# Performance work log

Measured on AMD Instinct MI355X. Metric: run time of the kernel, lower is better.

Reference implementation:

```python
import jax, jax.numpy as jnp
import numpy as np

N, IN_F, OUT_F, H = 8192, 256, 64, 4
NEG_SLOPE = 0.2


def setup_inputs() -> dict:
    key = jax.random.key(0)
    ks = jax.random.split(key, 8)
    inputs = jax.random.normal(ks[0], (N, IN_F), dtype=jnp.float32)
    # sparse-ish binary adjacency with self loops (sparse.softmax only sees nonzeros)
    adj = (jax.random.uniform(ks[1], (N, N)) < 0.05).astype(jnp.float32)
    idx = jnp.arange(N)
    adj = adj.at[idx, idx].set(1.0)
    stdv = 1.0 / np.sqrt(H * OUT_F)
    weight = jax.random.uniform(ks[2], (IN_F, H * OUT_F), minval=-stdv, maxval=stdv, dtype=jnp.float32)
    bias = jax.random.uniform(ks[3], (1, H * OUT_F), minval=-stdv, maxval=stdv, dtype=jnp.float32)
    # weight_u/v: stdv = 1/sqrt(size(-1)=1) = 1
    weight_u = jax.random.uniform(ks[4], (H, OUT_F, 1), minval=-1.0, maxval=1.0, dtype=jnp.float32)
    weight_v = jax.random.uniform(ks[5], (H, OUT_F, 1), minval=-1.0, maxval=1.0, dtype=jnp.float32)
    stdp = 1.0 / np.sqrt(IN_F)
    proj_w = jax.random.uniform(ks[6], (H * OUT_F, IN_F), minval=-stdp, maxval=stdp, dtype=jnp.float32)
    proj_b = jax.random.uniform(ks[7], (H * OUT_F,), minval=-stdp, maxval=stdp, dtype=jnp.float32)
    return {"inputs": inputs, "adj_mat": adj, "weight": weight, "weight_u": weight_u,
            "weight_v": weight_v, "bias": bias, "proj_w": proj_w, "proj_b": proj_b}


def reference(inputs, adj_mat, weight, weight_u, weight_v, bias, proj_w, proj_b):
    n = inputs.shape[0]
    support = (inputs @ weight).reshape(n, H, OUT_F).transpose(1, 0, 2)  # [H,N,O]
    f1 = jnp.einsum('hno,ho->hn', support, weight_u[..., 0])  # [H,N]
    f2 = jnp.einsum('hno,ho->hn', support, weight_v[..., 0])  # [H,N]
    logits = f1[:, None, :] + f2[:, :, None]                  # [H,N,N]
    w = jax.nn.leaky_relu(logits, NEG_SLOPE)
    masked = w * adj_mat                                      # adj broadcast over heads
    mask = adj_mat != 0.0
    # sparse.softmax over dim 2: softmax restricted to nonzero (edge) positions
    neg = jnp.where(mask, masked, -jnp.inf)
    m = jnp.max(neg, axis=2, keepdims=True)
    m = jnp.where(jnp.isfinite(m), m, 0.0)
    e = jnp.where(mask, jnp.exp(neg - m), 0.0)
    denom = jnp.sum(e, axis=2, keepdims=True)
    attn = e / jnp.where(denom > 0, denom, 1.0)               # [H,N,N]
    out = jnp.einsum('hnm,hmo->hno', attn, support)           # [H,N,O]
    out = out.transpose(1, 0, 2).reshape(n, H * OUT_F)
    out = out + bias
    out = out + inputs @ proj_w.T + proj_b
    return out
```

## Files before the change

### kernel.cpp

```cpp
#include <hip/hip_runtime.h>
#include <hip/hip_bf16.h>

#define N_NODES 8192
#define IN_FEAT 256
#define OUT_F   64
#define NHEAD   4
#define HF      256
#define NEG     0.2f

typedef unsigned short u16;
typedef unsigned char  u8;
typedef unsigned int   u32;
typedef unsigned long long u64;
typedef _Float16 h2    __attribute__((ext_vector_type(2)));
typedef _Float16 half8 __attribute__((ext_vector_type(8)));
typedef __attribute__((ext_vector_type(4))) float f32x4;

__global__ __launch_bounds__(256) void k_x16(const float* __restrict__ inp,
                                             _Float16* __restrict__ X16,
                                             float* __restrict__ anum,
                                             float* __restrict__ aden) {
    const int i = blockIdx.x * 256 + threadIdx.x;
    const float4 v = ((const float4*)inp)[i];
    union { _Float16 hh[4]; u64 q; } cv;
    cv.hh[0] = (_Float16)v.x; cv.hh[1] = (_Float16)v.y;
    cv.hh[2] = (_Float16)v.z; cv.hh[3] = (_Float16)v.w;
    ((u64*)X16)[i] = cv.q;
    ((float4*)anum)[i] = (float4){0.f, 0.f, 0.f, 0.f};
    if (i < 8192) ((float4*)aden)[i] = (float4){0.f, 0.f, 0.f, 0.f};
}

__global__ __launch_bounds__(256) void k_wpack(const float* __restrict__ W,
                                               const float* __restrict__ PW,
                                               _Float16* __restrict__ W16B) {
    const int w = blockIdx.x * 256 + threadIdx.x;
    const int ks = w >> 11;
    const int T  = (w >> 6) & 31;
    const int lane = w & 63;
    const int q  = lane >> 4, cc = lane & 15;
    const int n  = T * 16 + cc;
    const int k0 = ks * 32 + q * 8;
    union { _Float16 hh[8]; half8 v; } o;
    #pragma unroll
    for (int e = 0; e < 8; ++e) {
        const int k = k0 + e;
        const float s = (n < 256) ? W[k * 256 + n] : PW[(size_t)(n - 256) * 256 + k];
        o.hh[e] = (_Float16)s;
    }
    *(half8*)(W16B + (size_t)w * 8) = o.v;
}

__global__ __launch_bounds__(256) void k_bits(const float* __restrict__ adj,
                                              u64* __restrict__ gb64) {
    const int row  = blockIdx.x * 4 + (threadIdx.x >> 6);
    const int lane = threadIdx.x & 63;
    const float* ar = adj + (size_t)row * N_NODES;
    u64* gr = gb64 + (size_t)row * 128;
    #pragma unroll 1
    for (int it = 0; it < 32; ++it) {
        const int jb = it * 256;
        const float a0 = ar[jb + lane];
        const float a1 = ar[jb + 64 + lane];
        const float a2 = ar[jb + 128 + lane];
        const float a3 = ar[jb + 192 + lane];
        const u64 b0 = __ballot(a0 != 0.f);
        const u64 b1 = __ballot(a1 != 0.f);
        const u64 b2 = __ballot(a2 != 0.f);
        const u64 b3 = __ballot(a3 != 0.f);
        if (lane == 0) {
            gr[it * 4 + 0] = b0; gr[it * 4 + 1] = b1;
            gr[it * 4 + 2] = b2; gr[it * 4 + 3] = b3;
        }
    }
}

#define GROWS 16
__global__ __launch_bounds__(256) void k_gemm(
    const _Float16* __restrict__ X16,
    const _Float16* __restrict__ W16B,
    const float* __restrict__ U,
    const float* __restrict__ V,
    const float* __restrict__ Bias,
    const float* __restrict__ PB,
    _Float16* __restrict__ suppB,
    float* __restrict__ f1,
    float* __restrict__ f2,
    float* __restrict__ outp)
{
    __shared__ __align__(16) _Float16 xl[GROWS][264];
    const int n0  = blockIdx.x * GROWS;
    const int tid = threadIdx.x;
    const int wv  = tid >> 6, lane = tid & 63;
    const int col = lane & 15, quad = lane >> 4;

    {
        const int r = tid >> 4, seg = tid & 15;
        const half8* src = (const half8*)(X16 + (size_t)(n0 + r) * 256 + seg * 16);
        *(half8*)&xl[r][seg * 16]     = src[0];
        *(half8*)&xl[r][seg * 16 + 8] = src[1];
    }
    __syncthreads();

    f32x4 acc[8];
    #pragma unroll
    for (int t = 0; t < 8; ++t) acc[t] = (f32x4){0.f, 0.f, 0.f, 0.f};

    const int qo = quad * 8;
    #pragma unroll
    for (int ks = 0; ks < 8; ++ks) {
        const half8 af = *(const half8*)&xl[col][ks * 32 + qo];
        const _Float16* bb = W16B + ((size_t)(ks * 32 + wv * 8) * 64 + lane) * 8;
        #pragma unroll
        for (int t = 0; t < 8; ++t) {
            const half8 bw = *(const half8*)(bb + (size_t)t * 512);
            acc[t] = __builtin_amdgcn_mfma_f32_16x16x32_f16(af, bw, acc[t], 0, 0, 0);
        }
    }

    if (wv < 2) {
        const int jbg = n0 >> 5;
        const int nlo = n0 & 31;
        #pragma unroll
        for (int t = 0; t < 8; ++t) {
            const int cg = wv * 128 + t * 16 + col;
            const int h  = cg >> 6;
            const int tp = (cg >> 4) & 3;
            #pragma unroll
            for (int reg = 0; reg < 4; ++reg) {
                const int irow = quad * 4 + reg;
                const int j31  = nlo + irow;
                const size_t word = ((size_t)(h * 256 + jbg) * 4 + tp) * 64
                                  + ((j31 >> 3) << 4) + col;
                suppB[word * 8 + (j31 & 7)] = (_Float16)acc[t][reg];
            }
        }
        float s1a[4] = {0,0,0,0}, s2a[4] = {0,0,0,0};
        float s1b[4] = {0,0,0,0}, s2b[4] = {0,0,0,0};
        #pragma unroll
        for (int t = 0; t < 8; ++t) {
            const int cg = wv * 128 + t * 16 + col;
            const float uu = U[cg], vv = V[cg];
            #pragma unroll
            for (int reg = 0; reg < 4; ++reg) {
                if (t < 4) { s1a[reg] += acc[t][reg] * uu; s2a[reg] += acc[t][reg] * vv; }
                else       { s1b[reg] += acc[t][reg] * uu; s2b[reg] += acc[t][reg] * vv; }
            }
        }
        #pragma unroll
        for (int m = 1; m < 16; m <<= 1) {
            #pragma unroll
            for (int reg = 0; reg < 4; ++reg) {
                s1a[reg] += __shfl_xor(s1a[reg], m);
                s2a[reg] += __shfl_xor(s2a[reg], m);
                s1b[reg] += __shfl_xor(s1b[reg], m);
                s2b[reg] += __shfl_xor(s2b[reg], m);
            }
        }
        if (col == 0) {
            const int hA = wv * 2, hB = wv * 2 + 1;
            #pragma unroll
            for (int reg = 0; reg < 4; ++reg) {
                const int n = n0 + quad * 4 + reg;
                f1[hA * N_NODES + n] = s1a[reg];
                f2[hA * N_NODES + n] = s2a[reg];
                f1[hB * N_NODES + n] = s1b[reg];
                f2[hB * N_NODES + n] = s2b[reg];
            }
        }
    } else {
        #pragma unroll
        for (int t = 0; t < 8; ++t) {
            const int cg = (wv - 2) * 128 + t * 16 + col;
            const float bb2 = Bias[cg] + PB[cg];
            #pragma unroll
            for (int reg = 0; reg < 4; ++reg) {
                const int irow = quad * 4 + reg;
                outp[(size_t)(n0 + irow) * HF + cg] = acc[t][reg] + bb2;
            }
        }
    }
}

__global__ __launch_bounds__(256) void k_prep(const float* __restrict__ f1,
                                              float* __restrict__ f1max,
                                              _Float16* __restrict__ EA16,
                                              _Float16* __restrict__ EB16) {
    __shared__ float red[256];
    const int h = blockIdx.x;
    float m = -1e30f;
    for (int j = threadIdx.x; j < N_NODES; j += 256)
        m = fmaxf(m, f1[h * N_NODES + j]);
    red[threadIdx.x] = m;
    __syncthreads();
    for (int s = 128; s > 0; s >>= 1) {
        if (threadIdx.x < s) red[threadIdx.x] = fmaxf(red[threadIdx.x], red[threadIdx.x + s]);
        __syncthreads();
    }
    const float fm = red[0];
    if (threadIdx.x == 0) f1max[h] = fm;
    for (int j = threadIdx.x; j < N_NODES; j += 256) {
        const float d = f1[h * N_NODES + j] - fm;
        EA16[(size_t)h * N_NODES + j] = (_Float16)__expf(d);
        EB16[(size_t)h * N_NODES + j] = (_Float16)__expf(NEG * d);
    }
}

#define TI 64
#define NSUB 4
#define JSPLIT_G 4
#define JW (N_NODES / JSPLIT_G)

__global__ __launch_bounds__(256, 3) void k_attn_mfma(
    const unsigned* __restrict__ gb32,
    const _Float16* __restrict__ suppB,
    const _Float16* __restrict__ EA16,
    const _Float16* __restrict__ EB16,
    const float* __restrict__ f2,
    const float* __restrict__ f1max,
    float* __restrict__ anum,
    float* __restrict__ aden)
{
    __shared__ __align__(16) _Float16 ea_lds[NHEAD][JW];
    __shared__ __align__(16) _Float16 eb_lds[NHEAD][JW];
    __shared__ __align__(4)  u8 abyte[TI][260];

    const int itile = blockIdx.x >> 2;
    const int jwin  = blockIdx.x & 3;
    const int i0    = itile * TI;
    const int J0    = jwin * JW;
    const int wv    = threadIdx.x >> 6;
    const int lane  = threadIdx.x & 63;
    const int col   = lane & 15;
    const int quad  = lane >> 4;

    {
        const _Float16* gea = EA16 + (size_t)wv * N_NODES + J0;
        const _Float16* geb = EB16 + (size_t)wv * N_NODES + J0;
        #pragma unroll
        for (int it = 0; it < 4; ++it) {
            const int off = it * 512 + lane * 8;
            *(float4*)&ea_lds[wv][off] = *(const float4*)(gea + off);
            *(float4*)&eb_lds[wv][off] = *(const float4*)(geb + off);
        }
    }
    #pragma unroll
    for (int rr = 0; rr < 16; ++rr) {
        const int r = (wv << 4) + rr;
        *(unsigned*)&abyte[r][lane * 4] =
            gb32[(size_t)(i0 + r) * 256 + (J0 >> 5) + lane];
    }
    __syncthreads();

    const int h = wv;
    const float fm = f1max[h];
    h2 caH[NSUB], cbH[NSUB];
    float ls[NSUB];
    #pragma unroll
    for (int s = 0; s < NSUB; ++s) {
        const float f2i = f2[(size_t)h * N_NODES + i0 + s * 16 + col];
        const float g  = fm + f2i;
        const float mi = fmaxf(g, NEG * g);
        const _Float16 ca = (_Float16)__expf(g - mi);
        const _Float16 cb = (_Float16)__expf(NEG * g - mi);
        caH[s][0] = ca; caH[s][1] = ca;
        cbH[s][0] = cb; cbH[s][1] = cb;
        ls[s] = 0.f;
    }
    const h2 ones = {(_Float16)1.0f, (_Float16)1.0f};

    const _Float16* sb = suppB + (size_t)h * 524288
                       + (size_t)(J0 >> 5) * 2048 + lane * 8;

    f32x4 acc[NSUB][4];
    #pragma unroll
    for (int s = 0; s < NSUB; ++s)
        #pragma unroll
        for (int t = 0; t < 4; ++t)
            acc[s][t] = (f32x4){0.f, 0.f, 0.f, 0.f};

    const int qo = quad << 3;

    #pragma unroll 2
    for (int jb = 0; jb < JW; jb += 32) {
        const int jl = jb + qo;
        const _Float16* fp = sb + (size_t)(jb >> 5) * 2048;
        const half8 bv0 = *(const half8*)(fp);
        const half8 bv1 = *(const half8*)(fp + 512);
        const half8 bv2 = *(const half8*)(fp + 1024);
        const half8 bv3 = *(const half8*)(fp + 1536);

        union { half8 v; h2 pr[4]; } ea, eb;
        ea.v = *(const half8*)&ea_lds[h][jl];
        eb.v = *(const half8*)&eb_lds[h][jl];
        const int wo = (jb >> 3) + quad;

        #pragma unroll
        for (int s = 0; s < NSUB; ++s) {
            const unsigned gw = abyte[col + s * 16][wo];
            union { half8 v; unsigned w[4]; h2 pr[4]; } af;
            #pragma unroll
            for (int p = 0; p < 4; ++p) {
                const h2 pa = ea.pr[p] * caH[s];
                const h2 pb = eb.pr[p] * cbH[s];
                const h2 x  = __builtin_elementwise_max(pa, pb);
                const unsigned mlo = (unsigned)((int)(gw << (31 - 2 * p)) >> 31) & 0x0000FFFFu;
                const unsigned mhi = (unsigned)((int)(gw << (30 - 2 * p)) >> 31) & 0xFFFF0000u;
                union { h2 hh; unsigned u; } xu;
                xu.hh = x;
                xu.u &= (mlo | mhi);
                af.w[p] = xu.u;
                ls[s] = __builtin_amdgcn_fdot2(xu.hh, ones, ls[s], false);
            }
            acc[s][0] = __builtin_amdgcn_mfma_f32_16x16x32_f16(af.v, bv0, acc[s][0], 0, 0, 0);
            acc[s][1] = __builtin_amdgcn_mfma_f32_16x16x32_f16(af.v, bv1, acc[s][1], 0, 0, 0);
            acc[s][2] = __builtin_amdgcn_mfma_f32_16x16x32_f16(af.v, bv2, acc[s][2], 0, 0, 0);
            acc[s][3] = __builtin_amdgcn_mfma_f32_16x16x32_f16(af.v, bv3, acc[s][3], 0, 0, 0);
        }
    }

    #pragma unroll
    for (int s = 0; s < NSUB; ++s) {
        ls[s] += __shfl_xor(ls[s], 16);
        ls[s] += __shfl_xor(ls[s], 32);
    }
    if (quad == 0) {
        #pragma unroll
        for (int s = 0; s < NSUB; ++s)
            unsafeAtomicAdd(aden + (size_t)h * N_NODES + i0 + s * 16 + col, ls[s]);
    }

    #pragma unroll
    for (int s = 0; s < NSUB; ++s) {
        #pragma unroll
        for (int reg = 0; reg < 4; ++reg) {
            const int irow = (quad << 2) + reg;
            float* ap = anum + (size_t)(i0 + s * 16 + irow) * HF + (h << 6) + col;
            #pragma unroll
            for (int t = 0; t < 4; ++t)
                unsafeAtomicAdd(ap + (t << 4), acc[s][t][reg]);
        }
    }
}

__global__ __launch_bounds__(256) void k_fin(const float* __restrict__ anum,
                                             const float* __restrict__ aden,
                                             float* __restrict__ out) {
    const int c = threadIdx.x;
    const int h = c >> 6;
    #pragma unroll
    for (int rr = 0; rr < 4; ++rr) {
        const int n = blockIdx.x * 4 + rr;
        out[(size_t)n * HF + c] += anum[(size_t)n * HF + c]
                                 / aden[(size_t)h * N_NODES + n];
    }
}

extern "C" void kernel_launch(void* const* d_in, const int* in_sizes, int n_in,
                              void* d_out, int out_size, void* d_ws, size_t ws_size,
                              hipStream_t stream) {
    const float* inp  = (const float*)d_in[0];
    const float* adj  = (const float*)d_in[1];
    const float* W    = (const float*)d_in[2];
    const float* U    = (const float*)d_in[3];
    const float* V    = (const float*)d_in[4];
    const float* Bias = (const float*)d_in[5];
    const float* PW   = (const float*)d_in[6];
    const float* PB   = (const float*)d_in[7];
    float* out = (float*)d_out;

    char* ws = (char*)d_ws;
    _Float16* suppB = (_Float16*)(ws);
    float* f1    = (float*)(ws + (4u << 20));
    float* f2    = (float*)(ws + (4u << 20) + (128u << 10));
    float* f1mx  = (float*)(ws + (4u << 20) + (256u << 10));
    _Float16* EA16 = (_Float16*)(ws + (4u << 20) + (576u << 10));
    _Float16* EB16 = (_Float16*)(ws + (4u << 20) + (704u << 10));
    float* aden  = (float*)(ws + (4u << 20) + (832u << 10));
    u64*   gb64  = (u64*)(ws + (8u << 20));
    _Float16* X16  = (_Float16*)(ws + (16u << 20));
    _Float16* W16B = (_Float16*)(ws + (20u << 20));
    float* anum  = (float*)(ws + (24u << 20));

    k_x16  <<<2048, 256, 0, stream>>>(inp, X16, anum, aden);
    k_wpack<<<  64, 256, 0, stream>>>(W, PW, W16B);
    k_bits <<<2048, 256, 0, stream>>>(adj, gb64);
    k_gemm <<< 512, 256, 0, stream>>>(X16, W16B, U, V, Bias, PB,
                                      suppB, f1, f2, out);
    k_prep <<<NHEAD, 256, 0, stream>>>(f1, f1mx, EA16, EB16);
    k_attn_mfma<<<(N_NODES / TI) * JSPLIT_G, 256, 0, stream>>>(
        (const unsigned*)gb64, suppB, EA16, EB16, f2, f1mx, anum, aden);
    k_fin  <<<N_NODES / 4, 256, 0, stream>>>(anum, aden, out);
}
```

Before: 487.8 us.

## Fuse adjacency bitpacking into attention kernel and merge prep kernels

Removes the separate k_bits pass and instead has the attention kernel read the fp32 adjacency rows directly, building the per-tile bitmask with float4 loads. It also folds the weight-packing kernel into the input conversion kernel, and packs four fp16 suppB values into one 64-bit store in the GEMM epilogue. The aim is to avoid an extra 256MB adjacency read plus the bitmask write and read, and to cut kernel launches. The cost is that each thread in the attention prologue issues strided 128B-per-lane loads, which may stall the tile setup.

After: 469.5 us. 1.04x faster.

```diff
diff --git a/kernel.cpp b/kernel.cpp
--- a/kernel.cpp
+++ b/kernel.cpp
@@ -16,8 +16,11 @@
 typedef _Float16 half8 __attribute__((ext_vector_type(8)));
 typedef __attribute__((ext_vector_type(4))) float f32x4;
 
-__global__ __launch_bounds__(256) void k_x16(const float* __restrict__ inp,
+__global__ __launch_bounds__(256) void k_pre(const float* __restrict__ inp,
+                                             const float* __restrict__ W,
+                                             const float* __restrict__ PW,
                                              _Float16* __restrict__ X16,
+                                             _Float16* __restrict__ W16B,
                                              float* __restrict__ anum,
                                              float* __restrict__ aden) {
     const int i = blockIdx.x * 256 + threadIdx.x;
@@ -28,49 +31,23 @@
     ((u64*)X16)[i] = cv.q;
     ((float4*)anum)[i] = (float4){0.f, 0.f, 0.f, 0.f};
     if (i < 8192) ((float4*)aden)[i] = (float4){0.f, 0.f, 0.f, 0.f};
-}
-
-__global__ __launch_bounds__(256) void k_wpack(const float* __restrict__ W,
-                                               const float* __restrict__ PW,
-                                               _Float16* __restrict__ W16B) {
-    const int w = blockIdx.x * 256 + threadIdx.x;
-    const int ks = w >> 11;
-    const int T  = (w >> 6) & 31;
-    const int lane = w & 63;
-    const int q  = lane >> 4, cc = lane & 15;
-    const int n  = T * 16 + cc;
-    const int k0 = ks * 32 + q * 8;
-    union { _Float16 hh[8]; half8 v; } o;
-    #pragma unroll
-    for (int e = 0; e < 8; ++e) {
-        const int k = k0 + e;
-        const float s = (n < 256) ? W[k * 256 + n] : PW[(size_t)(n - 256) * 256 + k];
-        o.hh[e] = (_Float16)s;
-    }
-    *(half8*)(W16B + (size_t)w * 8) = o.v;
-}
-
-__global__ __launch_bounds__(256) void k_bits(const float* __restrict__ adj,
-                                              u64* __restrict__ gb64) {
-    const int row  = blockIdx.x * 4 + (threadIdx.x >> 6);
-    const int lane = threadIdx.x & 63;
-    const float* ar = adj + (size_t)row * N_NODES;
-    u64* gr = gb64 + (size_t)row * 128;
-    #pragma unroll 1
-    for (int it = 0; it < 32; ++it) {
-        const int jb = it * 256;
-        const float a0 = ar[jb + lane];
-        const float a1 = ar[jb + 64 + lane];
-        const float a2 = ar[jb + 128 + lane];
-        const float a3 = ar[jb + 192 + lane];
-        const u64 b0 = __ballot(a0 != 0.f);
-        const u64 b1 = __ballot(a1 != 0.f);
-        const u64 b2 = __ballot(a2 != 0.f);
-        const u64 b3 = __ballot(a3 != 0.f);
-        if (lane == 0) {
-            gr[it * 4 + 0] = b0; gr[it * 4 + 1] = b1;
-            gr[it * 4 + 2] = b2; gr[it * 4 + 3] = b3;
-        }
+
+    if (i < 16384) {
+        const int ks = i >> 11;
+        const int T  = (i >> 6) & 31;
+        const int lane = i & 63;
+        const int q  = lane >> 4, cc = lane & 15;
+        const int n  = T * 16 + cc;
+        const int k0 = ks * 32 + q * 8;
+        union { _Float16 hh[8]; half8 v8; } o;
+        #pragma unroll
+        for (int e = 0; e < 8; ++e) {
+            const int k = k0 + e;
+            const float s = (n < 256) ? W[k * 256 + n]
+                                      : PW[(size_t)(n - 256) * 256 + k];
+            o.hh[e] = (_Float16)s;
+        }
+        *(half8*)(W16B + (size_t)i * 8) = o.v8;
     }
 }
 
@@ -118,21 +95,21 @@
     }
 
     if (wv < 2) {
-        const int jbg = n0 >> 5;
-        const int nlo = n0 & 31;
+        const int jbg  = n0 >> 5;
+        const int nlo  = n0 & 31;
+        const int jq   = nlo + quad * 4;
+        const int e0   = jq & 7;
+        const int wrow = (jq >> 3) << 4;
         #pragma unroll
         for (int t = 0; t < 8; ++t) {
             const int cg = wv * 128 + t * 16 + col;
             const int h  = cg >> 6;
             const int tp = (cg >> 4) & 3;
-            #pragma unroll
-            for (int reg = 0; reg < 4; ++reg) {
-                const int irow = quad * 4 + reg;
-                const int j31  = nlo + irow;
-                const size_t word = ((size_t)(h * 256 + jbg) * 4 + tp) * 64
-                                  + ((j31 >> 3) << 4) + col;
-                suppB[word * 8 + (j31 & 7)] = (_Float16)acc[t][reg];
-            }
+            union { _Float16 hh[4]; u64 q; } pk;
+            #pragma unroll
+            for (int reg = 0; reg < 4; ++reg) pk.hh[reg] = (_Float16)acc[t][reg];
+            const size_t word = ((size_t)(h * 256 + jbg) * 4 + tp) * 64 + wrow + col;
+            *(u64*)(suppB + word * 8 + e0) = pk.q;
         }
         float s1a[4] = {0,0,0,0}, s2a[4] = {0,0,0,0};
         float s1b[4] = {0,0,0,0}, s2b[4] = {0,0,0,0};
@@ -211,7 +188,7 @@
 #define JW (N_NODES / JSPLIT_G)
 
 __global__ __launch_bounds__(256, 3) void k_attn_mfma(
-    const unsigned* __restrict__ gb32,
+    const float* __restrict__ adj,
     const _Float16* __restrict__ suppB,
     const _Float16* __restrict__ EA16,
     const _Float16* __restrict__ EB16,
@@ -243,11 +220,20 @@
             *(float4*)&eb_lds[wv][off] = *(const float4*)(geb + off);
         }
     }
-    #pragma unroll
+    #pragma unroll 2
     for (int rr = 0; rr < 16; ++rr) {
         const int r = (wv << 4) + rr;
-        *(unsigned*)&abyte[r][lane * 4] =
-            gb32[(size_t)(i0 + r) * 256 + (J0 >> 5) + lane];
+        const float* ar = adj + (size_t)(i0 + r) * N_NODES + J0 + lane * 32;
+        unsigned wrd = 0;
+        #pragma unroll
+        for (int p = 0; p < 8; ++p) {
+            const float4 a = *(const float4*)(ar + p * 4);
+            const unsigned nib =
+                (unsigned)(a.x != 0.f)        | ((unsigned)(a.y != 0.f) << 1) |
+                ((unsigned)(a.z != 0.f) << 2) | ((unsigned)(a.w != 0.f) << 3);
+            wrd |= nib << (p * 4);
+        }
+        *(unsigned*)&abyte[r][lane * 4] = wrd;
     }
     __syncthreads();
 
@@ -376,18 +362,15 @@
     _Float16* EA16 = (_Float16*)(ws + (4u << 20) + (576u << 10));
     _Float16* EB16 = (_Float16*)(ws + (4u << 20) + (704u << 10));
     float* aden  = (float*)(ws + (4u << 20) + (832u << 10));
-    u64*   gb64  = (u64*)(ws + (8u << 20));
     _Float16* X16  = (_Float16*)(ws + (16u << 20));
     _Float16* W16B = (_Float16*)(ws + (20u << 20));
     float* anum  = (float*)(ws + (24u << 20));
 
-    k_x16  <<<2048, 256, 0, stream>>>(inp, X16, anum, aden);
-    k_wpack<<<  64, 256, 0, stream>>>(W, PW, W16B);
-    k_bits <<<2048, 256, 0, stream>>>(adj, gb64);
+    k_pre  <<<2048, 256, 0, stream>>>(inp, W, PW, X16, W16B, anum, aden);
     k_gemm <<< 512, 256, 0, stream>>>(X16, W16B, U, V, Bias, PB,
                                       suppB, f1, f2, out);
     k_prep <<<NHEAD, 256, 0, stream>>>(f1, f1mx, EA16, EB16);
     k_attn_mfma<<<(N_NODES / TI) * JSPLIT_G, 256, 0, stream>>>(
-        (const unsigned*)gb64, suppB, EA16, EB16, f2, f1mx, anum, aden);
+        adj, suppB, EA16, EB16, f2, f1mx, anum, aden);
     k_fin  <<<N_NODES / 4, 256, 0, stream>>>(anum, aden, out);
 }
```
